# Optimization experiments

Measured on AMD Instinct MI355X. Metric: run time of the kernel, lower is better.

Reference implementation:

```python
import jax, jax.numpy as jnp
import numpy as np

B, L, D, N = 4, 2048, 1024, 16


def setup_inputs() -> dict:
    key = jax.random.key(0)
    ks = jax.random.split(key, 12)
    s = 1.0 / np.sqrt(D)
    inp = {
        'x': jax.random.normal(ks[0], (B, L, D), jnp.float32),
        'ln_g': jnp.ones((D,), jnp.float32),
        'ln_b': jnp.zeros((D,), jnp.float32),
        'w1_w': jax.random.normal(ks[1], (D, D), jnp.float32) * s,
        'w1_b': jnp.zeros((D,), jnp.float32),
        'v1_w': jax.random.normal(ks[2], (D, D), jnp.float32) * s,
        'v1_b': jnp.zeros((D,), jnp.float32),
        'w2_w': jax.random.normal(ks[3], (D, D), jnp.float32) * s,
        'w2_b': jnp.zeros((D,), jnp.float32),
        'conv_w': jax.random.normal(ks[4], (D, 1, 3), jnp.float32) * (1.0 / np.sqrt(3.0)),
        'A_log': jnp.log(jnp.broadcast_to(jnp.arange(1, N + 1, dtype=jnp.float32), (D, N))),
        'D_skip': jnp.ones((D,), jnp.float32),
        'W_dt': jax.random.normal(ks[5], (D, D), jnp.float32) * (s * 0.1),
        'b_dt': jnp.full((D,), -4.0, jnp.float32),
        'W_B': jax.random.normal(ks[6], (D, N), jnp.float32) * s,
        'W_C': jax.random.normal(ks[7], (D, N), jnp.float32) * s,
    }
    return inp


def _layernorm(x, g, b, eps=1e-5):
    mu = jnp.mean(x, axis=-1, keepdims=True)
    var = jnp.mean(jnp.square(x - mu), axis=-1, keepdims=True)
    return (x - mu) * jax.lax.rsqrt(var + eps) * g + b


def _silu(x):
    return x * jax.nn.sigmoid(x)


def _depthwise_conv(x, w):
    # x: (B, L, D), w: (D, 1, 3), padding=1, groups=D
    xc = x.transpose(0, 2, 1)  # (B, D, L)
    y = jax.lax.conv_general_dilated(
        xc, w, window_strides=(1,), padding=[(1, 1)],
        feature_group_count=xc.shape[1],
        dimension_numbers=('NCH', 'OIH', 'NCH'))
    return y.transpose(0, 2, 1)


def _selective_scan(u, A_log, D_skip, W_dt, b_dt, W_B, W_C):
    # u: (B, L, D) -> y: (B, L, D); diagonal selective SSM (Mamba S6)
    A = -jnp.exp(A_log)                              # (D, N)
    dt = jax.nn.softplus(u @ W_dt + b_dt)            # (B, L, D)
    Bt = u @ W_B                                     # (B, L, N)
    Ct = u @ W_C                                     # (B, L, N)

    def step(h, inp):
        dt_t, B_t, C_t, u_t = inp                    # (B,D),(B,N),(B,N),(B,D)
        dA = jnp.exp(dt_t[..., None] * A)            # (B, D, N)
        h = dA * h + (dt_t * u_t)[..., None] * B_t[:, None, :]
        y = jnp.einsum('bdn,bn->bd', h, C_t)
        return h, y

    h0 = jnp.zeros((u.shape[0], u.shape[2], A.shape[1]), u.dtype)
    xs = (dt.transpose(1, 0, 2), Bt.transpose(1, 0, 2),
          Ct.transpose(1, 0, 2), u.transpose(1, 0, 2))
    _, ys = jax.lax.scan(step, h0, xs)               # ys: (L, B, D)
    return ys.transpose(1, 0, 2) + u * D_skip


def reference(x, ln_g, ln_b, w1_w, w1_b, v1_w, v1_b, w2_w, w2_b, conv_w,
              A_log, D_skip, W_dt, b_dt, W_B, W_C):
    x_norm = _layernorm(x, ln_g, ln_b)
    x1 = x_norm @ w1_w + w1_b
    x_conv = _silu(_depthwise_conv(x1, conv_w))
    x_ssm = _selective_scan(x_conv, A_log, D_skip, W_dt, b_dt, W_B, W_C)
    v = _silu(x_norm @ v1_w + v1_b)
    return (x_ssm * v) @ w2_w + w2_b
```

## Files before the change

kernel.cpp:

```cpp
#include <hip/hip_runtime.h>
#include <hip/hip_bf16.h>

#define BB 4
#define LL 2048
#define DD 1024
#define NN 16
#define BL (BB * LL)
#define NC 64
#define LC 32
#define MB 1048576

typedef float f32x4 __attribute__((ext_vector_type(4)));
typedef __bf16 bf16x8 __attribute__((ext_vector_type(8)));

typedef __attribute__((address_space(1))) unsigned int as1_u32;
typedef __attribute__((address_space(3))) unsigned int as3_u32;

__device__ __forceinline__ void gl_lds16(const void* g, void* l) {
  __builtin_amdgcn_global_load_lds((as1_u32*)g, (as3_u32*)l, 16, 0, 0);
}

__device__ __forceinline__ float fast_sigmoid(float x) {
  return 1.f / (1.f + __expf(-x));
}

__global__ __launch_bounds__(256) void k_prep_ln(const float* __restrict__ w1,
                                                 const float* __restrict__ v1,
                                                 const float* __restrict__ wdt,
                                                 const float* __restrict__ w2,
                                                 const float* __restrict__ WB,
                                                 const float* __restrict__ WC,
                                                 __hip_bfloat16* __restrict__ wcat,
                                                 __hip_bfloat16* __restrict__ wdtbc,
                                                 __hip_bfloat16* __restrict__ w2T,
                                                 const float* __restrict__ x,
                                                 const float* __restrict__ ln_g,
                                                 const float* __restrict__ ln_b,
                                                 __hip_bfloat16* __restrict__ xnorm) {
  const int z = blockIdx.z;
  __shared__ float tile[32][33];
  __shared__ float red[8];
  if (z < 4) {
    const float* src = (z == 0) ? w1 : (z == 1) ? v1 : (z == 2) ? wdt : w2;
    __hip_bfloat16* dst = (z == 0) ? wcat
                        : (z == 1) ? (wcat + (size_t)1024 * DD)
                        : (z == 2) ? wdtbc : w2T;
    const int kt = blockIdx.x * 32, nt = blockIdx.y * 32;
    const int tx = threadIdx.x & 31, ty = threadIdx.x >> 5;
#pragma unroll
    for (int j = 0; j < 32; j += 8)
      tile[ty + j][tx] = src[(size_t)(kt + ty + j) * DD + nt + tx];
    __syncthreads();
#pragma unroll
    for (int j = 0; j < 32; j += 8)
      dst[(size_t)(nt + ty + j) * DD + kt + tx] = __float2bfloat16(tile[tx][ty + j]);
  } else if (z == 4) {
    const int id = blockIdx.y * 32 + blockIdx.x;
    if (id < 128) {
      const int idx = id * 256 + threadIdx.x;
      const int k = idx & 1023, n = idx >> 10;
      const float v = (n < 16) ? WB[(size_t)k * 16 + n] : WC[(size_t)k * 16 + (n - 16)];
      wdtbc[(size_t)(1024 + n) * DD + k] = __float2bfloat16(v);
    } else if (id < 512) {
      const int idx = (id - 128) * 256 + threadIdx.x;
      wdtbc[(size_t)1056 * DD + idx] = __float2bfloat16(0.f);
    }
  } else {
    const int row = (z - 5) * 1024 + blockIdx.y * 32 + blockIdx.x;
    const int tid = threadIdx.x;
    const f32x4 xv = *(const f32x4*)(x + (size_t)row * DD + tid * 4);
    float s = xv[0] + xv[1] + xv[2] + xv[3];
    float sq = xv[0] * xv[0] + xv[1] * xv[1] + xv[2] * xv[2] + xv[3] * xv[3];
#pragma unroll
    for (int o = 32; o > 0; o >>= 1) {
      s += __shfl_down(s, o);
      sq += __shfl_down(sq, o);
    }
    const int wave = tid >> 6, lane = tid & 63;
    if (lane == 0) { red[wave] = s; red[4 + wave] = sq; }
    __syncthreads();
    s = red[0] + red[1] + red[2] + red[3];
    sq = red[4] + red[5] + red[6] + red[7];
    const float mean = s * (1.f / DD);
    const float var = sq * (1.f / DD) - mean * mean;
    const float rs = rsqrtf(var + 1e-5f);
    const f32x4 gv = *(const f32x4*)(ln_g + tid * 4);
    const f32x4 bv = *(const f32x4*)(ln_b + tid * 4);
    union { ushort4 u; __hip_bfloat16 h[4]; } cv;
#pragma unroll
    for (int j = 0; j < 4; ++j)
      cv.h[j] = __float2bfloat16((xv[j] - mean) * rs * gv[j] + bv[j]);
    *reinterpret_cast<ushort4*>(&xnorm[(size_t)row * DD + tid * 4]) = cv.u;
  }
}

template <int EPI>
__device__ __forceinline__ void gemm_body(const __hip_bfloat16* __restrict__ Ag,
                                          const __hip_bfloat16* __restrict__ Wg,
                                          void* __restrict__ o0, void* __restrict__ o1,
                                          void* __restrict__ o2,
                                          const float* __restrict__ bias0,
                                          const float* __restrict__ bias1) {
  __shared__ unsigned short As[128 * 64];
  __shared__ unsigned short Bs[128 * 64];
  const int tid = threadIdx.x;
  const int wave = tid >> 6, lane = tid & 63;
  const int quad = lane >> 4, l16 = lane & 15;
  const int wm = wave & 1, wn = wave >> 1;

  const int srow = lane >> 3;
  const int schunk = (lane & 7) ^ srow;
  const char* gA = (const char*)Ag +
      (size_t)(blockIdx.x * 128 + wave * 32 + srow) * 2048 + schunk * 16;
  const char* gB = (const char*)Wg +
      (size_t)(blockIdx.y * 128 + wave * 32 + srow) * 2048 + schunk * 16;
  char* lA = (char*)As + wave * 32 * 128;
  char* lB = (char*)Bs + wave * 32 * 128;

  f32x4 acc[4][4] = {};

  for (int kt = 0; kt < 16; ++kt) {
#pragma unroll
    for (int i = 0; i < 4; ++i) {
      gl_lds16(gA + i * 8 * 2048, lA + i * 1024);
      gl_lds16(gB + i * 8 * 2048, lB + i * 1024);
    }
    gA += 128;
    gB += 128;
    __syncthreads();
    bf16x8 af[2][4], bfr[2][4];
#pragma unroll
    for (int h = 0; h < 2; ++h)
#pragma unroll
      for (int i = 0; i < 4; ++i) {
        const int ra = wm * 64 + i * 16 + l16;
        const int rb = wn * 64 + i * 16 + l16;
        af[h][i] = *(const bf16x8*)((const char*)As + ra * 128 +
                                    (((h * 4 + quad) ^ (ra & 7)) * 16));
        bfr[h][i] = *(const bf16x8*)((const char*)Bs + rb * 128 +
                                     (((h * 4 + quad) ^ (rb & 7)) * 16));
      }
#pragma unroll
    for (int h = 0; h < 2; ++h)
#pragma unroll
      for (int i = 0; i < 4; ++i)
#pragma unroll
        for (int j = 0; j < 4; ++j)
          acc[i][j] =
              __builtin_amdgcn_mfma_f32_16x16x32_bf16(af[h][i], bfr[h][j], acc[i][j], 0, 0, 0);
    __syncthreads();
  }

  const int em0 = blockIdx.x * 128 + wm * 64 + quad * 4;
  const int en0 = blockIdx.y * 128 + wn * 64 + l16;
#pragma unroll
  for (int i = 0; i < 4; ++i) {
#pragma unroll
    for (int r = 0; r < 4; ++r) {
      const int m = em0 + i * 16 + r;
#pragma unroll
      for (int j = 0; j < 4; ++j) {
        const int n = en0 + j * 16;
        const float val = acc[i][j][r];
        if constexpr (EPI == 1) {
          if (n < 1024) {
            ((__hip_bfloat16*)o0)[(size_t)m * DD + n] = __float2bfloat16(val + bias0[n]);
          } else {
            const float t = val + bias1[n - 1024];
            ((__hip_bfloat16*)o1)[(size_t)m * DD + (n - 1024)] =
                __float2bfloat16(t * fast_sigmoid(t));
          }
        } else if constexpr (EPI == 2) {
          if (n < 1024) {
            const float t = val + bias0[n];
            const float sp = (t > 15.f) ? t : __logf(1.f + __expf(t));
            ((__hip_bfloat16*)o0)[(size_t)m * DD + n] = __float2bfloat16(sp);
          } else if (n < 1040) {
            ((float*)o1)[(size_t)m * NN + (n - 1024)] = val;
          } else if (n < 1056) {
            ((float*)o2)[(size_t)m * NN + (n - 1040)] = val;
          }
        } else {
          ((float*)o0)[(size_t)m * DD + n] = val + bias0[n];
        }
      }
    }
  }
}

__global__ __launch_bounds__(256) void k_gemm_xv(const __hip_bfloat16* __restrict__ Ag,
                                                 const __hip_bfloat16* __restrict__ Wg,
                                                 void* o0, void* o1,
                                                 const float* __restrict__ b0,
                                                 const float* __restrict__ b1) {
  gemm_body<1>(Ag, Wg, o0, o1, nullptr, b0, b1);
}
__global__ __launch_bounds__(256) void k_gemm_dbc(const __hip_bfloat16* __restrict__ Ag,
                                                  const __hip_bfloat16* __restrict__ Wg,
                                                  void* o0, void* o1, void* o2,
                                                  const float* __restrict__ b0) {
  gemm_body<2>(Ag, Wg, o0, o1, o2, b0, nullptr);
}
__global__ __launch_bounds__(256) void k_gemm_out(const __hip_bfloat16* __restrict__ Ag,
                                                  const __hip_bfloat16* __restrict__ Wg,
                                                  void* o0, const float* __restrict__ b0) {
  gemm_body<3>(Ag, Wg, o0, nullptr, nullptr, b0, nullptr);
}

__global__ __launch_bounds__(256) void k_conv_silu(const __hip_bfloat16* __restrict__ x1,
                                                   const float* __restrict__ w,
                                                   __hip_bfloat16* __restrict__ out) {
  const size_t e = ((size_t)blockIdx.x * 256 + threadIdx.x) * 8;
  const int d = (int)(e & 1023);
  const int l = (int)((e >> 10) & 2047);
  const bf16x8 zero = {};
  const bf16x8 xm = (l > 0) ? *(const bf16x8*)(x1 + e - DD) : zero;
  const bf16x8 x0 = *(const bf16x8*)(x1 + e);
  const bf16x8 xp = (l < LL - 1) ? *(const bf16x8*)(x1 + e + DD) : zero;
  union { f32x4 v4[6]; float f[24]; } W;
  const f32x4* wp = (const f32x4*)(w + d * 3);
#pragma unroll
  for (int q = 0; q < 6; ++q) W.v4[q] = wp[q];
  bf16x8 o;
#pragma unroll
  for (int j = 0; j < 8; ++j) {
    const float a =
        W.f[j * 3 + 0] * (float)xm[j] + W.f[j * 3 + 1] * (float)x0[j] + W.f[j * 3 + 2] * (float)xp[j];
    o[j] = (__bf16)(a * fast_sigmoid(a));
  }
  *(bf16x8*)(out + e) = o;
}


__global__ __launch_bounds__(256) void k_scan1(const __hip_bfloat16* __restrict__ dt,
                                               const __hip_bfloat16* __restrict__ u,
                                               const float* __restrict__ Bt,
                                               const float* __restrict__ A_log,
                                               float* __restrict__ SD,
                                               float* __restrict__ hend) {
  const int d = blockIdx.x * 256 + threadIdx.x;
  const int c = blockIdx.y, b = blockIdx.z;
  __shared__ float Bsh[LC * NN];
  if (threadIdx.x < LC * NN / 4)
    ((f32x4*)Bsh)[threadIdx.x] =
        ((const f32x4*)(Bt + (size_t)(b * LL + c * LC) * NN))[threadIdx.x];
  float a[NN];
#pragma unroll
  for (int n = 0; n < NN; ++n) a[n] = -__expf(A_log[(size_t)d * NN + n]);
  const float a0 = a[0];
  bool pw = true;
#pragma unroll
  for (int n = 0; n < NN; ++n) pw &= (fabsf(a[n] - (n + 1) * a0) <= 1e-3f * (n + 1));
  __syncthreads();
  float h[NN] = {};
  float sdt = 0.f;
  size_t idx = (size_t)(b * LL + c * LC) * DD + d;
  if (pw) {
#pragma unroll 2
    for (int t = 0; t < LC; ++t, idx += DD) {
      const float dtv = __bfloat162float(dt[idx]);
      const float uv = __bfloat162float(u[idx]);
      sdt += dtv;
      const float du = dtv * uv;
      float w[NN];
      w[0] = __expf(dtv * a0);
#pragma unroll
      for (int n = 1; n < NN; ++n) w[n] = w[(n - 1) >> 1] * w[n >> 1];
#pragma unroll
      for (int n = 0; n < NN; ++n) h[n] = w[n] * h[n] + du * Bsh[t * NN + n];
    }
  } else {
#pragma unroll 2
    for (int t = 0; t < LC; ++t, idx += DD) {
      const float dtv = __bfloat162float(dt[idx]);
      const float uv = __bfloat162float(u[idx]);
      sdt += dtv;
      const float du = dtv * uv;
#pragma unroll
      for (int n = 0; n < NN; ++n)
        h[n] = __expf(dtv * a[n]) * h[n] + du * Bsh[t * NN + n];
    }
  }
  const size_t o = ((size_t)((b * NC + c) * DD + d)) * NN;
  SD[(size_t)(b * NC + c) * DD + d] = sdt;
#pragma unroll
  for (int n = 0; n < NN; ++n) hend[o + n] = h[n];
}

__global__ __launch_bounds__(256) void k_scan2(const float* __restrict__ SD,
                                               const float* __restrict__ A_log,
                                               float* __restrict__ h) {
  const int gidx = blockIdx.x * 256 + threadIdx.x;
  const int n = gidx & 15, d = (gidx >> 4) & 1023, b = gidx >> 14;
  const float an = -__expf(A_log[(size_t)d * NN + n]);
  float hs = 0.f;
  size_t off = ((size_t)b * NC * DD + d) * NN + n;
  size_t soff = (size_t)b * NC * DD + d;
  const size_t stride = (size_t)DD * NN;
  for (int c = 0; c < NC; ++c, off += stride, soff += DD) {
    const float he = h[off];
    const float p = __expf(SD[soff] * an);
    h[off] = hs;
    hs = p * hs + he;
  }
}

__global__ __launch_bounds__(256) void k_scan3(const __hip_bfloat16* __restrict__ dt,
                                               const __hip_bfloat16* __restrict__ u,
                                               const float* __restrict__ Bt,
                                               const float* __restrict__ Ct,
                                               const float* __restrict__ A_log,
                                               const float* __restrict__ hstart,
                                               const float* __restrict__ Dskip,
                                               const __hip_bfloat16* __restrict__ v,
                                               __hip_bfloat16* __restrict__ yA) {
  const int d = blockIdx.x * 256 + threadIdx.x;
  const int c = blockIdx.y, b = blockIdx.z;
  __shared__ float Bsh[LC * NN];
  __shared__ float Csh[LC * NN];
  if (threadIdx.x < 128)
    ((f32x4*)Bsh)[threadIdx.x] =
        ((const f32x4*)(Bt + (size_t)(b * LL + c * LC) * NN))[threadIdx.x];
  else
    ((f32x4*)Csh)[threadIdx.x - 128] =
        ((const f32x4*)(Ct + (size_t)(b * LL + c * LC) * NN))[threadIdx.x - 128];
  float a[NN];
#pragma unroll
  for (int n = 0; n < NN; ++n) a[n] = -__expf(A_log[(size_t)d * NN + n]);
  const float a0 = a[0];
  bool pw = true;
#pragma unroll
  for (int n = 0; n < NN; ++n) pw &= (fabsf(a[n] - (n + 1) * a0) <= 1e-3f * (n + 1));
  const float dsk = Dskip[d];
  float h[NN];
  const size_t o = ((size_t)((b * NC + c) * DD + d)) * NN;
#pragma unroll
  for (int n = 0; n < NN; ++n) h[n] = hstart[o + n];
  __syncthreads();
  size_t idx = (size_t)(b * LL + c * LC) * DD + d;
  if (pw) {
#pragma unroll 2
    for (int t = 0; t < LC; ++t, idx += DD) {
      const float dtv = __bfloat162float(dt[idx]);
      const float uv = __bfloat162float(u[idx]);
      const float du = dtv * uv;
      float w[NN];
      w[0] = __expf(dtv * a0);
#pragma unroll
      for (int n = 1; n < NN; ++n) w[n] = w[(n - 1) >> 1] * w[n >> 1];
      float y = 0.f;
#pragma unroll
      for (int n = 0; n < NN; ++n) {
        h[n] = w[n] * h[n] + du * Bsh[t * NN + n];
        y += h[n] * Csh[t * NN + n];
      }
      const float xssm = y + uv * dsk;
      const float vv = __bfloat162float(v[idx]);
      yA[idx] = __float2bfloat16(xssm * vv);
    }
  } else {
#pragma unroll 2
    for (int t = 0; t < LC; ++t, idx += DD) {
      const float dtv = __bfloat162float(dt[idx]);
      const float uv = __bfloat162float(u[idx]);
      const float du = dtv * uv;
      float y = 0.f;
#pragma unroll
      for (int n = 0; n < NN; ++n) {
        h[n] = __expf(dtv * a[n]) * h[n] + du * Bsh[t * NN + n];
        y += h[n] * Csh[t * NN + n];
      }
      const float xssm = y + uv * dsk;
      const float vv = __bfloat162float(v[idx]);
      yA[idx] = __float2bfloat16(xssm * vv);
    }
  }
}

extern "C" void kernel_launch(void* const* d_in, const int* in_sizes, int n_in,
                              void* d_out, int out_size, void* d_ws, size_t ws_size,
                              hipStream_t stream) {
  const float* x      = (const float*)d_in[0];
  const float* ln_g   = (const float*)d_in[1];
  const float* ln_b   = (const float*)d_in[2];
  const float* w1_w   = (const float*)d_in[3];
  const float* w1_b   = (const float*)d_in[4];
  const float* v1_w   = (const float*)d_in[5];
  const float* v1_b   = (const float*)d_in[6];
  const float* w2_w   = (const float*)d_in[7];
  const float* w2_b   = (const float*)d_in[8];
  const float* conv_w = (const float*)d_in[9];
  const float* A_log  = (const float*)d_in[10];
  const float* D_skip = (const float*)d_in[11];
  const float* W_dt   = (const float*)d_in[12];
  const float* b_dt   = (const float*)d_in[13];
  const float* W_B    = (const float*)d_in[14];
  const float* W_C    = (const float*)d_in[15];

  char* ws = (char*)d_ws;
  const size_t OFF_SLOTA = 0;
  const size_t OFF_SLOTB = (size_t)16 * MB;
  const size_t OFF_VBUF  = (size_t)32 * MB;
  const size_t OFF_YA    = (size_t)48 * MB;
  const size_t OFF_WCAT  = (size_t)64 * MB;
  const size_t OFF_WDTBC = (size_t)68 * MB;
  const size_t OFF_W2T   = OFF_WDTBC + 2359296;
  const size_t OFF_BT    = OFF_W2T + 2097152;
  const size_t OFF_CT    = OFF_BT + 524288;
  const size_t OFF_SD    = OFF_CT + 524288;
  const size_t OFF_H     = OFF_SD + 1048576;

  __hip_bfloat16* xnorm = (__hip_bfloat16*)(ws + OFF_SLOTA);
  __hip_bfloat16* xconv = (__hip_bfloat16*)(ws + OFF_SLOTA);
  __hip_bfloat16* x1    = (__hip_bfloat16*)(ws + OFF_SLOTB);
  __hip_bfloat16* dtb   = (__hip_bfloat16*)(ws + OFF_SLOTB);
  __hip_bfloat16* vbuf  = (__hip_bfloat16*)(ws + OFF_VBUF);
  __hip_bfloat16* yA    = (__hip_bfloat16*)(ws + OFF_YA);
  __hip_bfloat16* wcat  = (__hip_bfloat16*)(ws + OFF_WCAT);
  __hip_bfloat16* wdtbc = (__hip_bfloat16*)(ws + OFF_WDTBC);
  __hip_bfloat16* w2T   = (__hip_bfloat16*)(ws + OFF_W2T);
  float* Btf = (float*)(ws + OFF_BT);
  float* Ctf = (float*)(ws + OFF_CT);
  float* SD  = (float*)(ws + OFF_SD);
  float* H   = (float*)(ws + OFF_H);

  k_prep_ln<<<dim3(32, 32, 13), 256, 0, stream>>>(w1_w, v1_w, W_dt, w2_w, W_B, W_C,
                                                  wcat, wdtbc, w2T, x, ln_g, ln_b, xnorm);

  k_gemm_xv<<<dim3(BL / 128, 2048 / 128), 256, 0, stream>>>(
      xnorm, wcat, (void*)x1, (void*)vbuf, w1_b, v1_b);

  k_conv_silu<<<(BL * DD / 8) / 256, 256, 0, stream>>>(x1, conv_w, xconv);

  k_gemm_dbc<<<dim3(BL / 128, 1152 / 128), 256, 0, stream>>>(
      xconv, wdtbc, (void*)dtb, (void*)Btf, (void*)Ctf, b_dt);

  k_scan1<<<dim3(DD / 256, NC, BB), 256, 0, stream>>>(dtb, xconv, Btf, A_log, SD, H);
  k_scan2<<<(BB * DD * NN) / 256, 256, 0, stream>>>(SD, A_log, H);
  k_scan3<<<dim3(DD / 256, NC, BB), 256, 0, stream>>>(dtb, xconv, Btf, Ctf, A_log, H, D_skip,
                                                      vbuf, yA);

  k_gemm_out<<<dim3(BL / 128, 1024 / 128), 256, 0, stream>>>(yA, w2T, d_out, w2_b);
}
```

Before: 322.6 us.

## Double-buffer GEMM LDS tiles with K=32 stages to overlap loads and MFMA

Measured after the change: 337.4 us. 1.05x slower.

```diff
diff --git a/kernel.cpp b/kernel.cpp
--- a/kernel.cpp
+++ b/kernel.cpp
@@ -101,53 +101,70 @@
                                           void* __restrict__ o2,
                                           const float* __restrict__ bias0,
                                           const float* __restrict__ bias1) {
-  __shared__ unsigned short As[128 * 64];
-  __shared__ unsigned short Bs[128 * 64];
+  __shared__ unsigned short As0[128 * 32];
+  __shared__ unsigned short As1[128 * 32];
+  __shared__ unsigned short Bs0[128 * 32];
+  __shared__ unsigned short Bs1[128 * 32];
   const int tid = threadIdx.x;
   const int wave = tid >> 6, lane = tid & 63;
   const int quad = lane >> 4, l16 = lane & 15;
   const int wm = wave & 1, wn = wave >> 1;
 
-  const int srow = lane >> 3;
-  const int schunk = (lane & 7) ^ srow;
+  const int srow = lane >> 2;
+  const int schunk = (lane & 3) ^ (srow & 3);
   const char* gA = (const char*)Ag +
       (size_t)(blockIdx.x * 128 + wave * 32 + srow) * 2048 + schunk * 16;
   const char* gB = (const char*)Wg +
       (size_t)(blockIdx.y * 128 + wave * 32 + srow) * 2048 + schunk * 16;
-  char* lA = (char*)As + wave * 32 * 128;
-  char* lB = (char*)Bs + wave * 32 * 128;
+  char* lA0 = (char*)As0 + wave * 2048;
+  char* lA1 = (char*)As1 + wave * 2048;
+  char* lB0 = (char*)Bs0 + wave * 2048;
+  char* lB1 = (char*)Bs1 + wave * 2048;
 
   f32x4 acc[4][4] = {};
 
-  for (int kt = 0; kt < 16; ++kt) {
+  gl_lds16(gA, lA0);
+  gl_lds16(gA + 16 * 2048, lA0 + 1024);
+  gl_lds16(gB, lB0);
+  gl_lds16(gB + 16 * 2048, lB0 + 1024);
+  gA += 64;
+  gB += 64;
+  __syncthreads();
+
+  auto compute = [&](const unsigned short* Ab, const unsigned short* Bb) {
+    bf16x8 af[4], bfr[4];
 #pragma unroll
     for (int i = 0; i < 4; ++i) {
-      gl_lds16(gA + i * 8 * 2048, lA + i * 1024);
-      gl_lds16(gB + i * 8 * 2048, lB + i * 1024);
-    }
-    gA += 128;
-    gB += 128;
+      const int ra = wm * 64 + i * 16 + l16;
+      const int rb = wn * 64 + i * 16 + l16;
+      af[i] = *(const bf16x8*)((const char*)Ab + ra * 64 + ((quad ^ (ra & 3)) * 16));
+      bfr[i] = *(const bf16x8*)((const char*)Bb + rb * 64 + ((quad ^ (rb & 3)) * 16));
+    }
+#pragma unroll
+    for (int i = 0; i < 4; ++i)
+#pragma unroll
+      for (int j = 0; j < 4; ++j)
+        acc[i][j] = __builtin_amdgcn_mfma_f32_16x16x32_bf16(af[i], bfr[j], acc[i][j], 0, 0, 0);
+  };
+
+  for (int p = 0; p < 16; ++p) {
+    gl_lds16(gA, lA1);
+    gl_lds16(gA + 16 * 2048, lA1 + 1024);
+    gl_lds16(gB, lB1);
+    gl_lds16(gB + 16 * 2048, lB1 + 1024);
+    gA += 64;
+    gB += 64;
+    compute(As0, Bs0);
     __syncthreads();
-    bf16x8 af[2][4], bfr[2][4];
-#pragma unroll
-    for (int h = 0; h < 2; ++h)
-#pragma unroll
-      for (int i = 0; i < 4; ++i) {
-        const int ra = wm * 64 + i * 16 + l16;
-        const int rb = wn * 64 + i * 16 + l16;
-        af[h][i] = *(const bf16x8*)((const char*)As + ra * 128 +
-                                    (((h * 4 + quad) ^ (ra & 7)) * 16));
-        bfr[h][i] = *(const bf16x8*)((const char*)Bs + rb * 128 +
-                                     (((h * 4 + quad) ^ (rb & 7)) * 16));
-      }
-#pragma unroll
-    for (int h = 0; h < 2; ++h)
-#pragma unroll
-      for (int i = 0; i < 4; ++i)
-#pragma unroll
-        for (int j = 0; j < 4; ++j)
-          acc[i][j] =
-              __builtin_amdgcn_mfma_f32_16x16x32_bf16(af[h][i], bfr[h][j], acc[i][j], 0, 0, 0);
+    if (p < 15) {
+      gl_lds16(gA, lA0);
+      gl_lds16(gA + 16 * 2048, lA0 + 1024);
+      gl_lds16(gB, lB0);
+      gl_lds16(gB + 16 * 2048, lB0 + 1024);
+      gA += 64;
+      gB += 64;
+    }
+    compute(As1, Bs1);
     __syncthreads();
   }
 
```
